# Performance work log

Hardware: AMD Instinct MI355X
Metric: run time of the kernel (lower is better)

The kernel has to match this reference:

```python
import jax, jax.numpy as jnp
import numpy as np

BN_EPS = 0.001

def conv2d(x, w, b, stride, pad):
    # x: NCHW, w: OIHW
    y = jax.lax.conv_general_dilated(x, w, (stride, stride), [(pad, pad), (pad, pad)],
                                     dimension_numbers=('NCHW', 'OIHW', 'NCHW'))
    return y + b[None, :, None, None]

def up2(x):
    return jnp.repeat(jnp.repeat(x, 2, axis=2), 2, axis=3)

def bn_eval(x, g, b):
    # BatchNorm in eval mode with fresh running stats (mean=0, var=1)
    inv = g / jnp.sqrt(1.0 + BN_EPS)
    return inv[None, :, None, None] * x + b[None, :, None, None]

def setup_inputs() -> dict:
    key = jax.random.key(0)
    ks = jax.random.split(key, 16)
    inp = {}
    inp['x_init'] = jax.random.uniform(ks[0], (8, 3, 1024, 1024), dtype=jnp.float32)
    inp['thresh'] = jax.random.uniform(ks[1], (2,), dtype=jnp.float32)
    inp['sample_w'] = jax.random.normal(ks[2], (3, 3, 4, 4), dtype=jnp.float32) * 0.1
    inp['sample_b'] = jax.random.normal(ks[3], (3,), dtype=jnp.float32) * 0.1
    inp['centers'] = jax.random.uniform(ks[4], (8,), dtype=jnp.float32)
    inp['pool1_w'] = jax.random.normal(ks[5], (3, 3, 2, 2), dtype=jnp.float32) * 0.2
    inp['pool1_b'] = jax.random.normal(ks[6], (3,), dtype=jnp.float32) * 0.1
    inp['pool2_w'] = jax.random.normal(ks[7], (3, 3, 2, 2), dtype=jnp.float32) * 0.2
    inp['pool2_b'] = jax.random.normal(ks[8], (3,), dtype=jnp.float32) * 0.1
    inp['ctx_conv_w'] = jax.random.normal(ks[9], (4, 3, 3, 3, 3), dtype=jnp.float32) * 0.2
    inp['ctx_conv_b'] = jax.random.normal(ks[10], (4, 3), dtype=jnp.float32) * 0.1
    inp['ctx_bn_g'] = jax.random.uniform(ks[11], (4, 3), dtype=jnp.float32) + 0.5
    inp['ctx_bn_b'] = jax.random.normal(ks[12], (4, 3), dtype=jnp.float32) * 0.1
    return inp

def _quant_idx_counts(t, mask, centers):
    # counts[k] = #(elements of t with mask and argmin center == k)
    idx = jnp.argmin((t[..., None] - centers) ** 2, axis=-1)  # same shape as t
    oh = idx[..., None] == jnp.arange(centers.shape[0])
    return jnp.sum((mask[..., None] & oh).astype(jnp.float32), axis=(0, 1, 2, 3))

def reference(x_init, thresh, sample_w, sample_b, centers,
              pool1_w, pool1_b, pool2_w, pool2_b,
              ctx_conv_w, ctx_conv_b, ctx_bn_g, ctx_bn_b):
    # spectral norm of sample conv weight (exact largest singular value)
    sigma = jnp.linalg.svd(sample_w.reshape(sample_w.shape[0], -1), compute_uv=False)[0]
    x = conv2d(x_init, sample_w / sigma, sample_b, 4, 0)  # [B,3,H/4,W/4]
    B, C, H, W = x.shape

    # ContextExtractor: conv_i(relu(bn_i(h))), stride 2 each
    h = x_init
    for i in range(3):
        h = conv2d(jax.nn.relu(bn_eval(h, ctx_bn_g[i], ctx_bn_b[i])), ctx_conv_w[i], ctx_conv_b[i], 2, 1)
    h1 = conv2d(jax.nn.relu(bn_eval(h, ctx_bn_g[3], ctx_bn_b[3])), ctx_conv_w[3], ctx_conv_b[3], 2, 1)
    feat_1 = (jnp.tanh(h) + 1.0) / 2.0    # [B,3,H/8,W/8]
    feat_2 = (jnp.tanh(h1) + 1.0) / 2.0   # [B,3,H/16,W/16]

    th_1, th_2 = thresh[0], thresh[1]
    feat_1_ = up2(feat_1)
    feat_2_ = up2(up2(feat_2))

    p1 = conv2d(x, pool1_w, pool1_b, 2, 0)    # half res
    p2 = conv2d(p1, pool2_w, pool2_b, 2, 0)   # quarter res
    ss_1 = up2(p1)
    ss_2 = up2(up2(p2))

    cond_2 = feat_2_ < th_2
    cond_1 = jnp.logical_and(jnp.logical_not(cond_2), feat_1_ < th_1)
    cond_0 = jnp.logical_not(jnp.logical_or(cond_1, cond_2))
    mask_1 = jnp.logical_and(up2(feat_2) >= th_2, feat_1 < th_1)  # half-res mask for p1
    mask_2 = feat_2 < th_2                                         # quarter-res mask for p2

    xq = jnp.where(cond_1, ss_1, x)
    xq = jnp.where(cond_2, ss_2, xq)

    # soft vector quantization against 8 learned centers
    d = (xq[..., None] - centers) ** 2                 # [B,C,H,W,8]
    soft = jnp.sum(centers * jax.nn.softmax(-d, axis=-1), axis=-1)

    # compression statistics (esti_cr; huffman real_cr omitted - host-side, non-tensor)
    esti_size = (jnp.sum(cond_0.astype(jnp.float32))
                 + jnp.sum(cond_1.astype(jnp.float32)) / 4.0
                 + jnp.sum(cond_2.astype(jnp.float32)) / 16.0)
    esti_cr = (1.0 / 16.0) * esti_size / (H * W * C * B)

    # histogram std over comp_data quantization indices, via masked counts
    counts = (_quant_idx_counts(x, cond_0, centers)
              + _quant_idx_counts(p1, mask_1, centers)
              + _quant_idx_counts(p2, mask_2, centers))
    counts = counts / jnp.sum(counts)
    std = jnp.std(counts, ddof=1)

    return (soft, esti_cr, std)
```

## Files before the change

kernel.cpp:

```cpp
#include <hip/hip_runtime.h>
#include <math.h>


#define SENT -1e30f
#define SXSTR 72
#define SXCH  (19 * SXSTR)
#define H0STR 36
#define H0CH  (9 * H0STR)

__device__ __forceinline__ float featf(float h) { return 0.5f * (tanhf(h) + 1.0f); }

__device__ __forceinline__ void stage19(const float* __restrict__ base,
                                        float* __restrict__ L,
                                        int gr0, int gc0, int S, int t) {
    #pragma unroll
    for (int p = 0; p < 2; p++) {
        int idx = t + 256 * p;
        if (idx < 323) {
            int lr = idx / 17;
            int s  = idx - lr * 17;
            int gr = gr0 + lr;
            int gc = gc0 + 4 * s;
            float4 v;
            if (gr >= 0 && gr < S && gc >= 0 && gc < S)
                v = *(const float4*)(base + (size_t)gr * S + gc);
            else { v.x = SENT; v.y = SENT; v.z = SENT; v.w = SENT; }
            *(float4*)&L[lr * SXSTR + 4 * s] = v;
        }
    }
}

__global__ __launch_bounds__(256) void k_fused01(
    const float* __restrict__ xin,
    const float* __restrict__ sw_g, const float* __restrict__ sb,
    const float* __restrict__ ctxw, const float* __restrict__ ctxb,
    const float* __restrict__ bng, const float* __restrict__ bnb,
    const float* __restrict__ p1w, const float* __restrict__ p1b,
    const float* __restrict__ p2w, const float* __restrict__ p2b,
    float* __restrict__ outX, float* __restrict__ outH1,
    float* __restrict__ outP1, float* __restrict__ outP2)
{
    __shared__ float sx[3 * SXCH];
    __shared__ float sm[3 * H0CH];

    int t = threadIdx.x, bid = blockIdx.x;
    int tileX = bid & 15, bandY = (bid >> 4) & 63, b = bid >> 10;

    int gr0 = bandY * 16 - 3;
    int gc0 = tileX * 64 - 4;
    #pragma unroll
    for (int c = 0; c < 3; c++)
        stage19(xin + ((size_t)(b * 3 + c) << 20), &sx[c * SXCH], gr0, gc0, 1024, t);
    __syncthreads();

    {
        float inv0[3], bb0[3];
        #pragma unroll
        for (int c = 0; c < 3; c++) { inv0[c] = bng[c] / sqrtf(1.001f); bb0[c] = bnb[c]; }
        #pragma unroll
        for (int p = 0; p < 2; p++) {
            int idx = t + 256 * p;
            if (idx < 297) {
                int lhy = idx / 33;
                int lhx = idx - 33 * lhy;
                bool oob = (bandY == 0 && lhy == 0) || (tileX == 0 && lhx == 0);
                float a0 = ctxb[0], a1 = ctxb[1], a2 = ctxb[2];
                #pragma unroll
                for (int c = 0; c < 3; c++) {
                    const float* basep = &sx[c * SXCH + 2 * lhy * SXSTR + 2 * lhx];
                    float inv = inv0[c], bb = bb0[c];
                    #pragma unroll
                    for (int kh = 0; kh < 3; kh++) {
                        float2 c0 = *(const float2*)(basep + kh * SXSTR);
                        float2 c1 = *(const float2*)(basep + kh * SXSTR + 2);
                        float t0 = fmaxf(fmaf(inv, c0.y, bb), 0.0f);
                        float t1 = fmaxf(fmaf(inv, c1.x, bb), 0.0f);
                        float t2 = fmaxf(fmaf(inv, c1.y, bb), 0.0f);
                        int wi = c * 9 + kh * 3;
                        a0 = fmaf(ctxw[wi], t0, a0); a0 = fmaf(ctxw[wi + 1], t1, a0); a0 = fmaf(ctxw[wi + 2], t2, a0);
                        a1 = fmaf(ctxw[27 + wi], t0, a1); a1 = fmaf(ctxw[28 + wi], t1, a1); a1 = fmaf(ctxw[29 + wi], t2, a1);
                        a2 = fmaf(ctxw[54 + wi], t0, a2); a2 = fmaf(ctxw[55 + wi], t1, a2); a2 = fmaf(ctxw[56 + wi], t2, a2);
                    }
                }
                int o = lhy * H0STR + lhx;
                if (oob) { a0 = SENT; a1 = SENT; a2 = SENT; }
                sm[o] = a0; sm[H0CH + o] = a1; sm[2 * H0CH + o] = a2;
            }
        }
    }
    __syncthreads();

    if (t < 64) {
        int lx = t & 15, ly = t >> 4;
        const float* w1c = ctxw + 81;
        float a0 = ctxb[3], a1 = ctxb[4], a2 = ctxb[5];
        #pragma unroll
        for (int c = 0; c < 3; c++) {
            float inv = bng[3 + c] / sqrtf(1.001f), bb = bnb[3 + c];
            const float* mb = &sm[c * H0CH + 2 * ly * H0STR + 2 * lx];
            #pragma unroll
            for (int kh = 0; kh < 3; kh++) {
                float2 c0 = *(const float2*)(mb + kh * H0STR);
                float c2v = mb[kh * H0STR + 2];
                float t0 = fmaxf(fmaf(inv, c0.x, bb), 0.0f);
                float t1 = fmaxf(fmaf(inv, c0.y, bb), 0.0f);
                float t2 = fmaxf(fmaf(inv, c2v, bb), 0.0f);
                int wi = c * 9 + kh * 3;
                a0 = fmaf(w1c[wi], t0, a0); a0 = fmaf(w1c[wi + 1], t1, a0); a0 = fmaf(w1c[wi + 2], t2, a0);
                a1 = fmaf(w1c[27 + wi], t0, a1); a1 = fmaf(w1c[28 + wi], t1, a1); a1 = fmaf(w1c[29 + wi], t2, a1);
                a2 = fmaf(w1c[54 + wi], t0, a2); a2 = fmaf(w1c[55 + wi], t1, a2); a2 = fmaf(w1c[56 + wi], t2, a2);
            }
        }
        unsigned o = (unsigned)(b * 3) * 65536u + (unsigned)(bandY * 4 + ly) * 256u + tileX * 16 + lx;
        outH1[o] = a0; outH1[o + 65536u] = a1; outH1[o + 131072u] = a2;
    } else if (t < 128) {
        int tl = t - 64;
        float p00 = 0.f, p01 = 0.f, p02 = 0.f, p11 = 0.f, p12 = 0.f, p22 = 0.f;
        if (tl < 48) {
            float a0 = sw_g[tl], a1 = sw_g[48 + tl], a2 = sw_g[96 + tl];
            p00 = a0 * a0; p01 = a0 * a1; p02 = a0 * a2;
            p11 = a1 * a1; p12 = a1 * a2; p22 = a2 * a2;
        }
        #pragma unroll
        for (int off = 32; off > 0; off >>= 1) {
            p00 += __shfl_down(p00, off); p01 += __shfl_down(p01, off);
            p02 += __shfl_down(p02, off); p11 += __shfl_down(p11, off);
            p12 += __shfl_down(p12, off); p22 += __shfl_down(p22, off);
        }
        float inv_sigma = 0.0f;
        if (tl == 0) {
            float q = (p00 + p11 + p22) * (1.0f / 3.0f);
            float pp1 = p01 * p01 + p02 * p02 + p12 * p12;
            float pp2 = (p00 - q) * (p00 - q) + (p11 - q) * (p11 - q)
                      + (p22 - q) * (p22 - q) + 2.0f * pp1;
            float lam;
            if (pp2 < 1e-30f) lam = q;
            else {
                float pr = sqrtf(pp2 / 6.0f);
                float B00 = (p00 - q) / pr, B01 = p01 / pr, B02 = p02 / pr;
                float B11 = (p11 - q) / pr, B12 = p12 / pr, B22 = (p22 - q) / pr;
                float detB = B00 * (B11 * B22 - B12 * B12)
                           - B01 * (B01 * B22 - B12 * B02)
                           + B02 * (B01 * B12 - B11 * B02);
                float r = fminf(1.0f, fmaxf(-1.0f, 0.5f * detB));
                lam = q + 2.0f * pr * cosf(acosf(r) * (1.0f / 3.0f));
            }
            double G00 = p00, G01 = p01, G02 = p02, G11 = p11, G12 = p12, G22 = p22;
            double c2 = G00 + G11 + G22;
            double c1 = G00 * G11 - G01 * G01 + G00 * G22 - G02 * G02 + G11 * G22 - G12 * G12;
            double c0 = G00 * (G11 * G22 - G12 * G12) - G01 * (G01 * G22 - G12 * G02)
                      + G02 * (G01 * G12 - G11 * G02);
            double L = (double)lam;
            #pragma unroll
            for (int it = 0; it < 2; it++) {
                double pv = ((L - c2) * L + c1) * L - c0;
                double dv = (3.0 * L - 2.0 * c2) * L + c1;
                L -= pv / dv;
            }
            inv_sigma = (float)(1.0 / sqrt(L));
        }
        inv_sigma = __shfl(inv_sigma, 0);

        int xl = tl & 15, yl = tl >> 4;
        float4 r[3][4];
        #pragma unroll
        for (int c = 0; c < 3; c++)
            #pragma unroll
            for (int kh = 0; kh < 4; kh++)
                r[c][kh] = *(const float4*)&sx[c * SXCH + (4 * yl + 3 + kh) * SXSTR + 4 * xl + 4];
        float s0 = 0.f, s1 = 0.f, s2 = 0.f;
        #pragma unroll
        for (int c = 0; c < 3; c++)
            #pragma unroll
            for (int kh = 0; kh < 4; kh++) {
                float4 vv = r[c][kh];
                const float* w0 = &sw_g[(0 * 3 + c) * 16 + kh * 4];
                const float* w1 = &sw_g[(1 * 3 + c) * 16 + kh * 4];
                const float* w2 = &sw_g[(2 * 3 + c) * 16 + kh * 4];
                s0 += w0[0] * vv.x + w0[1] * vv.y + w0[2] * vv.z + w0[3] * vv.w;
                s1 += w1[0] * vv.x + w1[1] * vv.y + w1[2] * vv.z + w1[3] * vv.w;
                s2 += w2[0] * vv.x + w2[1] * vv.y + w2[2] * vv.z + w2[3] * vv.w;
            }
        float x0 = fmaf(s0, inv_sigma, sb[0]);
        float x1 = fmaf(s1, inv_sigma, sb[1]);
        float x2 = fmaf(s2, inv_sigma, sb[2]);
        unsigned o = (unsigned)(b * 3) * 65536u + (unsigned)(bandY * 4 + yl) * 256u + tileX * 16 + xl;
        outX[o] = x0; outX[o + 65536u] = x1; outX[o + 131072u] = x2;

        int sl = 2 * (tl & 7) + 32 * ((tl >> 3) & 1);
        float q0 = p1b[0], q1 = p1b[1], q2 = p1b[2];
        #pragma unroll
        for (int dy = 0; dy < 2; dy++)
            #pragma unroll
            for (int dx = 0; dx < 2; dx++) {
                int src = sl + dx + 16 * dy;
                float vx0 = __shfl(x0, src);
                float vx1 = __shfl(x1, src);
                float vx2 = __shfl(x2, src);
                int wi = dy * 2 + dx;
                q0 = fmaf(p1w[wi], vx0, q0); q0 = fmaf(p1w[4 + wi],  vx1, q0); q0 = fmaf(p1w[8 + wi],  vx2, q0);
                q1 = fmaf(p1w[12 + wi], vx0, q1); q1 = fmaf(p1w[16 + wi], vx1, q1); q1 = fmaf(p1w[20 + wi], vx2, q1);
                q2 = fmaf(p1w[24 + wi], vx0, q2); q2 = fmaf(p1w[28 + wi], vx1, q2); q2 = fmaf(p1w[32 + wi], vx2, q2);
            }
        if (tl < 16) {
            int px = tl & 7, py = tl >> 3;
            unsigned op = (unsigned)(b * 3) * 16384u + (unsigned)(bandY * 2 + py) * 128u + tileX * 8 + px;
            outP1[op] = q0; outP1[op + 16384u] = q1; outP1[op + 32768u] = q2;
        }

        int s2l = 2 * (tl & 3);
        float r0 = p2b[0], r1 = p2b[1], r2 = p2b[2];
        #pragma unroll
        for (int dy = 0; dy < 2; dy++)
            #pragma unroll
            for (int dx = 0; dx < 2; dx++) {
                int src = s2l + dx + 8 * dy;
                float vq0 = __shfl(q0, src);
                float vq1 = __shfl(q1, src);
                float vq2 = __shfl(q2, src);
                int wi = dy * 2 + dx;
                r0 = fmaf(p2w[wi], vq0, r0); r0 = fmaf(p2w[4 + wi],  vq1, r0); r0 = fmaf(p2w[8 + wi],  vq2, r0);
                r1 = fmaf(p2w[12 + wi], vq0, r1); r1 = fmaf(p2w[16 + wi], vq1, r1); r1 = fmaf(p2w[20 + wi], vq2, r1);
                r2 = fmaf(p2w[24 + wi], vq0, r2); r2 = fmaf(p2w[28 + wi], vq1, r2); r2 = fmaf(p2w[32 + wi], vq2, r2);
            }
        if (tl < 4) {
            unsigned op = (unsigned)(b * 3) * 4096u + (unsigned)bandY * 64u + tileX * 4 + tl;
            outP2[op] = r0; outP2[op + 4096u] = r1; outP2[op + 8192u] = r2;
        }
    }
}

__global__ __launch_bounds__(256) void k_fused23(
    const float* __restrict__ h1, float* __restrict__ outF1, float* __restrict__ outF2,
    const float* __restrict__ ctxw, const float* __restrict__ ctxb,
    const float* __restrict__ bng, const float* __restrict__ bnb)
{
    __shared__ float sx[3 * SXCH];
    __shared__ float sm[3 * H0CH];

    int t = threadIdx.x, bid = blockIdx.x;
    int tileX = bid & 3, bandY = (bid >> 2) & 15, b = bid >> 6;

    int gr0 = bandY * 16 - 3;
    int gc0 = tileX * 64 - 4;
    #pragma unroll
    for (int c = 0; c < 3; c++)
        stage19(h1 + (size_t)(b * 3 + c) * 65536, &sx[c * SXCH], gr0, gc0, 256, t);
    __syncthreads();

    {
        const float* w2c = ctxw + 162;
        float inv2[3], bb2[3];
        #pragma unroll
        for (int c = 0; c < 3; c++) { inv2[c] = bng[6 + c] / sqrtf(1.001f); bb2[c] = bnb[6 + c]; }
        #pragma unroll
        for (int p = 0; p < 2; p++) {
            int idx = t + 256 * p;
            if (idx < 297) {
                int lhy = idx / 33;
                int lhx = idx - 33 * lhy;
                bool oob = (bandY == 0 && lhy == 0) || (tileX == 0 && lhx == 0);
                float a0 = ctxb[6], a1 = ctxb[7], a2 = ctxb[8];
                #pragma unroll
                for (int c = 0; c < 3; c++) {
                    const float* basep = &sx[c * SXCH + 2 * lhy * SXSTR + 2 * lhx];
                    float inv = inv2[c], bb = bb2[c];
                    #pragma unroll
                    for (int kh = 0; kh < 3; kh++) {
                        float2 c0 = *(const float2*)(basep + kh * SXSTR);
                        float2 c1 = *(const float2*)(basep + kh * SXSTR + 2);
                        float t0 = fmaxf(fmaf(inv, c0.y, bb), 0.0f);
                        float t1 = fmaxf(fmaf(inv, c1.x, bb), 0.0f);
                        float t2 = fmaxf(fmaf(inv, c1.y, bb), 0.0f);
                        int wi = c * 9 + kh * 3;
                        a0 = fmaf(w2c[wi], t0, a0); a0 = fmaf(w2c[wi + 1], t1, a0); a0 = fmaf(w2c[wi + 2], t2, a0);
                        a1 = fmaf(w2c[27 + wi], t0, a1); a1 = fmaf(w2c[28 + wi], t1, a1); a1 = fmaf(w2c[29 + wi], t2, a1);
                        a2 = fmaf(w2c[54 + wi], t0, a2); a2 = fmaf(w2c[55 + wi], t1, a2); a2 = fmaf(w2c[56 + wi], t2, a2);
                    }
                }
                int o = lhy * H0STR + lhx;
                if (!oob && lhy >= 1 && lhx >= 1) {
                    unsigned fo = (unsigned)(b * 3) * 16384u
                                + (unsigned)(8 * bandY + lhy - 1) * 128u + 32 * tileX + lhx - 1;
                    outF1[fo] = featf(a0); outF1[fo + 16384u] = featf(a1); outF1[fo + 32768u] = featf(a2);
                }
                if (oob) { a0 = SENT; a1 = SENT; a2 = SENT; }
                sm[o] = a0; sm[H0CH + o] = a1; sm[2 * H0CH + o] = a2;
            }
        }
    }
    __syncthreads();

    if (t < 64) {
        int lx = t & 15, ly = t >> 4;
        const float* w3c = ctxw + 243;
        float a0 = ctxb[9], a1 = ctxb[10], a2 = ctxb[11];
        #pragma unroll
        for (int c = 0; c < 3; c++) {
            float inv = bng[9 + c] / sqrtf(1.001f), bb = bnb[9 + c];
            const float* mb = &sm[c * H0CH + 2 * ly * H0STR + 2 * lx];
            #pragma unroll
            for (int kh = 0; kh < 3; kh++) {
                float2 c0 = *(const float2*)(mb + kh * H0STR);
                float c2v = mb[kh * H0STR + 2];
                float t0 = fmaxf(fmaf(inv, c0.x, bb), 0.0f);
                float t1 = fmaxf(fmaf(inv, c0.y, bb), 0.0f);
                float t2 = fmaxf(fmaf(inv, c2v, bb), 0.0f);
                int wi = c * 9 + kh * 3;
                a0 = fmaf(w3c[wi], t0, a0); a0 = fmaf(w3c[wi + 1], t1, a0); a0 = fmaf(w3c[wi + 2], t2, a0);
                a1 = fmaf(w3c[27 + wi], t0, a1); a1 = fmaf(w3c[28 + wi], t1, a1); a1 = fmaf(w3c[29 + wi], t2, a1);
                a2 = fmaf(w3c[54 + wi], t0, a2); a2 = fmaf(w3c[55 + wi], t1, a2); a2 = fmaf(w3c[56 + wi], t2, a2);
            }
        }
        unsigned o = (unsigned)(b * 3) * 4096u + (unsigned)(bandY * 4 + ly) * 64u + tileX * 16 + lx;
        outF2[o] = featf(a0); outF2[o + 4096u] = featf(a1); outF2[o + 8192u] = featf(a2);
    }
}

__device__ __forceinline__ int argmin8(float v, const float* __restrict__ sc) {
    float best = 1e30f; int ki = 0;
    #pragma unroll
    for (int k = 0; k < 8; k++) {
        float df = v - sc[k]; float dk = df * df;
        if (dk < best) { best = dk; ki = k; }
    }
    return ki;
}

__global__ __launch_bounds__(256) void k_final(
    const float* __restrict__ x, const float* __restrict__ f1,
    const float* __restrict__ f2, const float* __restrict__ p1,
    const float* __restrict__ p2, const float* __restrict__ thresh,
    const float* __restrict__ centers, float* __restrict__ out,
    int* __restrict__ partials)
{
    __shared__ int sh[4 * 12];
    int t = threadIdx.x;
    int lane = t & 63;
    int* shW = &sh[12 * (t >> 6)];
    if (lane < 12) shW[lane] = 0;
    float sc[8];
    #pragma unroll
    for (int k = 0; k < 8; k++) sc[k] = centers[k];
    __syncthreads();

    float th1 = thresh[0], th2 = thresh[1];
    int gid = blockIdx.x * 256 + t;
    int xc = gid & 255, y = (gid >> 8) & 255, b = gid >> 16;
    unsigned i2 = (unsigned)(((y >> 1) << 7) + (xc >> 1));
    unsigned i4 = (unsigned)(((y >> 2) << 6) + (xc >> 2));
    bool doM1 = ((y & 1) == 0) && ((xc & 1) == 0);
    bool doM2 = ((y & 3) == 0) && ((xc & 3) == 0);
    int c0n = 0, c1n = 0, c2n = 0;

    #pragma unroll
    for (int c = 0; c < 3; c++) {
        unsigned pc = (unsigned)(b * 3 + c);
        float f1v = f1[pc * 16384u + i2];
        float f2v = f2[pc * 4096u + i4];
        float p1v = p1[pc * 16384u + i2];
        float p2v = p2[pc * 4096u + i4];
        float xv  = x[pc * 65536u + (unsigned)((y << 8) + xc)];
        bool cond2 = f2v < th2;
        bool cond1 = (!cond2) && (f1v < th1);
        bool cond0 = !(cond1 || cond2);
        float xq = cond2 ? p2v : (cond1 ? p1v : xv);

        float d[8]; float dmin = 1e30f;
        #pragma unroll
        for (int k = 0; k < 8; k++) { float df = xq - sc[k]; d[k] = df * df; dmin = fminf(dmin, d[k]); }
        float se = 0.f, sn = 0.f;
        #pragma unroll
        for (int k = 0; k < 8; k++) { float e = __expf(dmin - d[k]); se += e; sn = fmaf(sc[k], e, sn); }
        out[pc * 65536u + (unsigned)((y << 8) + xc)] = sn / se;

        c0n += cond0; c1n += cond1; c2n += cond2;

        if (cond0) atomicAdd(&shW[argmin8(xv, sc)], 1);
        if (doM1 && (f2v >= th2) && (f1v < th1)) atomicAdd(&shW[argmin8(p1v, sc)], 1);
        if (doM2 && cond2) atomicAdd(&shW[argmin8(p2v, sc)], 1);
    }
    #pragma unroll
    for (int off = 32; off > 0; off >>= 1) {
        c0n += __shfl_down(c0n, off);
        c1n += __shfl_down(c1n, off);
        c2n += __shfl_down(c2n, off);
    }
    if (lane == 0) { atomicAdd(&shW[8], c0n); atomicAdd(&shW[9], c1n); atomicAdd(&shW[10], c2n); }
    __syncthreads();
    if (t < 12)
        partials[blockIdx.x * 12 + t] = sh[t] + sh[12 + t] + sh[24 + t] + sh[36 + t];
}

__global__ void k_reduce(const int* __restrict__ partials, float* __restrict__ out2) {
    __shared__ int accs[12];
    int t = threadIdx.x;
    if (t < 12) accs[t] = 0;
    __syncthreads();
    int s[12];
    #pragma unroll
    for (int k = 0; k < 12; k++) s[k] = 0;
    for (int r = t; r < 2048; r += 256) {
        const int* row = partials + r * 12;
        #pragma unroll
        for (int k = 0; k < 12; k++) s[k] += row[k];
    }
    #pragma unroll
    for (int k = 0; k < 12; k++) {
        #pragma unroll
        for (int off = 32; off > 0; off >>= 1) s[k] += __shfl_down(s[k], off);
    }
    if ((t & 63) == 0) {
        #pragma unroll
        for (int k = 0; k < 12; k++) if (s[k]) atomicAdd(&accs[k], s[k]);
    }
    __syncthreads();
    if (t == 0) {
        float cnt0 = (float)accs[8], cnt1 = (float)accs[9], cnt2 = (float)accs[10];
        float esti = cnt0 + cnt1 * 0.25f + cnt2 * 0.0625f;
        float cr = (1.0f / 16.0f) * esti / (256.0f * 256.0f * 3.0f * 8.0f);
        float cs[8]; float tot = 0.0f;
        #pragma unroll
        for (int k = 0; k < 8; k++) { cs[k] = (float)accs[k]; tot += cs[k]; }
        float mean = 0.0f;
        #pragma unroll
        for (int k = 0; k < 8; k++) { cs[k] /= tot; mean += cs[k]; }
        mean *= 0.125f;
        float var = 0.0f;
        #pragma unroll
        for (int k = 0; k < 8; k++) { float df = cs[k] - mean; var += df * df; }
        var *= (1.0f / 7.0f);
        out2[0] = cr;
        out2[1] = sqrtf(var);
    }
}

extern "C" void kernel_launch(void* const* d_in, const int* in_sizes, int n_in,
                              void* d_out, int out_size, void* d_ws, size_t ws_size,
                              hipStream_t stream) {
    const float* x_init   = (const float*)d_in[0];
    const float* thresh   = (const float*)d_in[1];
    const float* sample_w = (const float*)d_in[2];
    const float* sample_b = (const float*)d_in[3];
    const float* centers  = (const float*)d_in[4];
    const float* pool1_w  = (const float*)d_in[5];
    const float* pool1_b  = (const float*)d_in[6];
    const float* pool2_w  = (const float*)d_in[7];
    const float* pool2_b  = (const float*)d_in[8];
    const float* ctx_w    = (const float*)d_in[9];
    const float* ctx_b    = (const float*)d_in[10];
    const float* bn_g     = (const float*)d_in[11];
    const float* bn_b     = (const float*)d_in[12];
    float* out = (float*)d_out;

    float* wsf      = (float*)d_ws;
    int*   partials = (int*)wsf;
    float* bufX     = wsf + 32768;
    float* bufH1    = bufX  + 1572864;
    float* bufP1    = bufH1 + 1572864;
    float* bufP2    = bufP1 + 393216;
    float* bufF1    = bufP2 + 98304;
    float* bufF2    = bufF1 + 393216;

    k_fused01<<<8192, 256, 0, stream>>>(x_init, sample_w, sample_b,
                                        ctx_w, ctx_b, bn_g, bn_b,
                                        pool1_w, pool1_b, pool2_w, pool2_b,
                                        bufX, bufH1, bufP1, bufP2);
    k_fused23<<<512, 256, 0, stream>>>(bufH1, bufF1, bufF2,
                                       ctx_w, ctx_b, bn_g, bn_b);
    k_final<<<2048, 256, 0, stream>>>(bufX, bufF1, bufF2, bufP1, bufP2,
                                      thresh, centers, out, partials);
    k_reduce<<<1, 256, 0, stream>>>(partials, out + 1572864);
}
```

Measured before the change: 213.0 us.

## Stage input tile into LDS via direct global-to-LDS loads

Replaces the register-staged float4 loads of the 19x68 input halo tile with __builtin_amdgcn_global_load_lds transfers that write straight into shared memory in a dense 68-float row layout. Out-of-bounds addresses are clamped, and a separate pass overwrites the top and left halo rows and columns with the sentinel for edge tiles. The goal is to skip the VGPR round-trip and cut load latency and register pressure. In exchange the row stride shrinks from 72 to 68, which may change LDS bank conflicts, and edge tiles pay an extra barrier.

```diff
diff --git a/kernel.cpp b/kernel.cpp
--- a/kernel.cpp
+++ b/kernel.cpp
@@ -3,12 +3,22 @@
 
 
 #define SENT -1e30f
+
+#define DSTR 68
+#define DPLANE 1292
+
 #define SXSTR 72
 #define SXCH  (19 * SXSTR)
 #define H0STR 36
 #define H0CH  (9 * H0STR)
 
 __device__ __forceinline__ float featf(float h) { return 0.5f * (tanhf(h) + 1.0f); }
+
+__device__ __forceinline__ void dma16(const float* g, float* l) {
+    __builtin_amdgcn_global_load_lds((const __attribute__((address_space(1))) void*)g,
+                                     (__attribute__((address_space(3))) void*)l,
+                                     16, 0, 0);
+}
 
 __device__ __forceinline__ void stage19(const float* __restrict__ base,
                                         float* __restrict__ L,
@@ -40,7 +50,7 @@
     float* __restrict__ outX, float* __restrict__ outH1,
     float* __restrict__ outP1, float* __restrict__ outP2)
 {
-    __shared__ float sx[3 * SXCH];
+    __shared__ float sx[3 * DPLANE];
     __shared__ float sm[3 * H0CH];
 
     int t = threadIdx.x, bid = blockIdx.x;
@@ -48,10 +58,42 @@
 
     int gr0 = bandY * 16 - 3;
     int gc0 = tileX * 64 - 4;
-    #pragma unroll
-    for (int c = 0; c < 3; c++)
-        stage19(xin + ((size_t)(b * 3 + c) << 20), &sx[c * SXCH], gr0, gc0, 1024, t);
-    __syncthreads();
+
+    {
+        int slot0 = t;
+        int lr0 = slot0 / 17, cs0 = slot0 - 17 * lr0;
+        int slot1 = t + 256;
+        int lr1 = slot1 / 17, cs1 = slot1 - 17 * lr1;
+        int grA = min(max(gr0 + lr0, 0), 1023);
+        int gcA = min(max(gc0 + 4 * cs0, 0), 1020);
+        int grB = min(max(gr0 + lr1, 0), 1023);
+        int gcB = min(max(gc0 + 4 * cs1, 0), 1020);
+        int offA = (grA << 10) + gcA;
+        int offB = (grB << 10) + gcB;
+        int wbase = t & 192;
+        #pragma unroll
+        for (int c = 0; c < 3; c++) {
+            const float* plane = xin + ((size_t)(b * 3 + c) << 20);
+            dma16(plane + offA, &sx[c * DPLANE + 4 * wbase]);
+            if (t < 67) dma16(plane + offB, &sx[c * DPLANE + 4 * (256 + wbase)]);
+        }
+    }
+    __syncthreads();
+
+    if (tileX == 0 || bandY == 0) {
+        float4 sv; sv.x = SENT; sv.y = SENT; sv.z = SENT; sv.w = SENT;
+        if (bandY == 0 && t < 153) {
+            int c = t / 51, rem = t - 51 * c;
+            int lr = rem / 17, cs = rem - 17 * lr;
+            *(float4*)&sx[c * DPLANE + lr * DSTR + 4 * cs] = sv;
+        }
+        if (tileX == 0 && t >= 192 && t < 249) {
+            int u = t - 192;
+            int c = u / 19, lr = u - 19 * c;
+            *(float4*)&sx[c * DPLANE + lr * DSTR] = sv;
+        }
+        __syncthreads();
+    }
 
     {
         float inv0[3], bb0[3];
@@ -67,12 +109,12 @@
                 float a0 = ctxb[0], a1 = ctxb[1], a2 = ctxb[2];
                 #pragma unroll
                 for (int c = 0; c < 3; c++) {
-                    const float* basep = &sx[c * SXCH + 2 * lhy * SXSTR + 2 * lhx];
+                    const float* basep = &sx[c * DPLANE + 2 * lhy * DSTR + 2 * lhx];
                     float inv = inv0[c], bb = bb0[c];
                     #pragma unroll
                     for (int kh = 0; kh < 3; kh++) {
-                        float2 c0 = *(const float2*)(basep + kh * SXSTR);
-                        float2 c1 = *(const float2*)(basep + kh * SXSTR + 2);
+                        float2 c0 = *(const float2*)(basep + kh * DSTR);
+                        float2 c1 = *(const float2*)(basep + kh * DSTR + 2);
                         float t0 = fmaxf(fmaf(inv, c0.y, bb), 0.0f);
                         float t1 = fmaxf(fmaf(inv, c1.x, bb), 0.0f);
                         float t2 = fmaxf(fmaf(inv, c1.y, bb), 0.0f);
@@ -167,7 +209,7 @@
         for (int c = 0; c < 3; c++)
             #pragma unroll
             for (int kh = 0; kh < 4; kh++)
-                r[c][kh] = *(const float4*)&sx[c * SXCH + (4 * yl + 3 + kh) * SXSTR + 4 * xl + 4];
+                r[c][kh] = *(const float4*)&sx[c * DPLANE + (4 * yl + 3 + kh) * DSTR + 4 * xl + 4];
         float s0 = 0.f, s1 = 0.f, s2 = 0.f;
         #pragma unroll
         for (int c = 0; c < 3; c++)
```

After: 206.5 us. -3.0%, faster.
